# Optimization experiments

Hardware: AMD Instinct MI355X
Metric: run time of the kernel (lower is better)

The kernel has to match this reference:

```python
import jax, jax.numpy as jnp
import numpy as np

N_NODES = 100000
N_GRAPHS = 1000
NPG = 100           # nodes per graph (fixed)
N_EDGES = 3200000   # avg degree 32
F_IN = 128
K = 30              # SortAggregation k
N_CLASSES = 10


def setup_inputs() -> dict:
    key = jax.random.key(0)
    ks = jax.random.split(key, 24)
    x = jax.random.normal(ks[0], (N_NODES, F_IN), jnp.float32)
    # edges constrained within each 100-node graph
    g = jax.random.randint(ks[1], (N_EDGES,), 0, N_GRAPHS)
    src = g * NPG + jax.random.randint(ks[2], (N_EDGES,), 0, NPG)
    dst = g * NPG + jax.random.randint(ks[3], (N_EDGES,), 0, NPG)
    edge_index = jnp.stack([src, dst]).astype(jnp.int32)
    batch = jnp.repeat(jnp.arange(N_GRAPHS, dtype=jnp.int32), NPG)

    def lin(k, fi, fo):
        return jax.random.normal(k, (fi, fo), jnp.float32) / np.sqrt(fi)

    return {
        "x": x, "edge_index": edge_index, "batch": batch,
        "W1": lin(ks[4], F_IN, 32), "b1": jnp.zeros((32,), jnp.float32),
        "W2": lin(ks[5], 32, 32),   "b2": jnp.zeros((32,), jnp.float32),
        "W3": lin(ks[6], 32, 32),   "b3": jnp.zeros((32,), jnp.float32),
        "W4": lin(ks[7], 32, 1),    "b4": jnp.zeros((1,), jnp.float32),
        "conv5_w": jax.random.normal(ks[8], (16, 1, 97), jnp.float32) / np.sqrt(97.0),
        "conv5_b": jnp.zeros((16,), jnp.float32),
        "conv6_w": jax.random.normal(ks[9], (32, 16, 5), jnp.float32) / np.sqrt(16 * 5.0),
        "conv6_b": jnp.zeros((32,), jnp.float32),
        "fc1_w": lin(ks[10], 352, 128), "fc1_b": jnp.zeros((128,), jnp.float32),
        "fc2_w": lin(ks[11], 128, N_CLASSES), "fc2_b": jnp.zeros((N_CLASSES,), jnp.float32),
    }


def reference(x, edge_index, batch,
              W1, b1, W2, b2, W3, b3, W4, b4,
              conv5_w, conv5_b, conv6_w, conv6_b,
              fc1_w, fc1_b, fc2_w, fc2_b):
    N = x.shape[0]
    src, dst = edge_index[0], edge_index[1]
    # remove_self_loops -> zero edge weight; GCNConv then re-adds self loops (weight 1)
    w = jnp.where(src == dst, 0.0, 1.0).astype(x.dtype)
    deg = jax.ops.segment_sum(w, dst, num_segments=N) + 1.0  # includes self loop
    dis = jax.lax.rsqrt(deg)
    norm = w * dis[src] * dis[dst]        # per-edge D^-1/2 A D^-1/2
    self_norm = dis * dis                 # self-loop coefficient 1/deg

    def gcn(h, W, b):
        h = h @ W                                   # [N, out]
        agg = jax.ops.segment_sum(norm[:, None] * h[src], dst, num_segments=N)
        return agg + self_norm[:, None] * h + b

    x1 = jnp.tanh(gcn(x, W1, b1))
    x2 = jnp.tanh(gcn(x1, W2, b2))
    x3 = jnp.tanh(gcn(x2, W3, b3))
    x4 = jnp.tanh(gcn(x3, W4, b4))
    h = jnp.concatenate([x1, x2, x3, x4], axis=-1)  # [N, 97]
    C = h.shape[-1]

    # SortAggregation(k=30): per graph, sort nodes by last channel descending, keep top k
    xs = h.reshape(N_GRAPHS, NPG, C)
    order = jnp.argsort(-xs[..., -1], axis=1)[:, :K]            # [B, K]
    pooled = jnp.take_along_axis(xs, order[:, :, None], axis=1)  # [B, K, C]
    y = pooled.reshape(N_GRAPHS, 1, K * C)                       # [B, 1, 2910]

    dn = ('NCH', 'OIH', 'NCH')
    y = jax.lax.conv_general_dilated(y, conv5_w, (97,), 'VALID', dimension_numbers=dn)
    y = jax.nn.relu(y + conv5_b[None, :, None])                  # [B, 16, 30]
    B, Co, L = y.shape
    y = y.reshape(B, Co, L // 2, 2).max(axis=-1)                 # maxpool(2,2) -> [B,16,15]
    y = jax.lax.conv_general_dilated(y, conv6_w, (1,), 'VALID', dimension_numbers=dn)
    y = jax.nn.relu(y + conv6_b[None, :, None])                  # [B, 32, 11]
    y = y.reshape(B, -1)                                         # [B, 352]
    out = jax.nn.relu(y @ fc1_w + fc1_b)                         # dropout = identity (eval)
    return jax.nn.log_softmax(out @ fc2_w + fc2_b, axis=-1)
```

## Files before the change

kernel.cpp:

```cpp
#include <hip/hip_runtime.h>

#define N_GRAPHS_C 1000
#define NPG_C      100
#define N_EDGES_C  3200000
#define KTOP_C     30
#define CAP        4096
#define NB_BUCKET  391

typedef _Float16 f16x8 __attribute__((ext_vector_type(8)));
typedef float    f32x4 __attribute__((ext_vector_type(4)));

__device__ __forceinline__ unsigned packh2(float x, float y) {
    _Float16 hx = (_Float16)x, hy = (_Float16)y;
    return (unsigned)__builtin_bit_cast(unsigned short, hx) |
           ((unsigned)__builtin_bit_cast(unsigned short, hy) << 16);
}

__device__ __forceinline__ float f16b(unsigned v) {
    return (float)__builtin_bit_cast(_Float16, (unsigned short)v);
}

__device__ __forceinline__ float ftanh(float x) {
    float e = __expf(2.0f * x);
    return 1.0f - 2.0f * __builtin_amdgcn_rcpf(e + 1.0f);
}

__device__ __forceinline__ void split8(const float* v, f16x8& h, f16x8& l) {
    #pragma unroll
    for (int j = 0; j < 8; ++j) {
        _Float16 hh = (_Float16)v[j];
        h[j] = hh;
        l[j] = (_Float16)(v[j] - (float)hh);
    }
}


__global__ __launch_bounds__(1024)
void bucket_kernel(const int* __restrict__ src, const int* __restrict__ dst,
                   int* __restrict__ gcur, unsigned short* __restrict__ slots,
                   const float* __restrict__ W1, const float* __restrict__ W2,
                   const float* __restrict__ W3, unsigned* __restrict__ wp) {
    const int tid = threadIdx.x;
    if (blockIdx.x == NB_BUCKET) {
        for (int w = tid; w < 2048; w += 1024) {
            int n = w >> 6, kp = w & 63, k = kp * 2;
            float a = W1[k*32 + n], b = W1[(k+1)*32 + n];
            _Float16 ah = (_Float16)a, bh = (_Float16)b;
            wp[w]        = (unsigned)__builtin_bit_cast(unsigned short, ah) |
                           ((unsigned)__builtin_bit_cast(unsigned short, bh) << 16);
            wp[2048 + w] = packh2(a - (float)ah, b - (float)bh);
        }
        for (int w = tid; w < 512; w += 1024) {
            int n = w >> 4, kp = w & 15, k = kp * 2;
            float a = W2[k*32 + n], b = W2[(k+1)*32 + n];
            _Float16 ah = (_Float16)a, bh = (_Float16)b;
            wp[4096 + w] = (unsigned)__builtin_bit_cast(unsigned short, ah) |
                           ((unsigned)__builtin_bit_cast(unsigned short, bh) << 16);
            wp[4608 + w] = packh2(a - (float)ah, b - (float)bh);
            float a3 = W3[k*32 + n], b3v = W3[(k+1)*32 + n];
            _Float16 a3h = (_Float16)a3, b3h = (_Float16)b3v;
            wp[5120 + w] = (unsigned)__builtin_bit_cast(unsigned short, a3h) |
                           ((unsigned)__builtin_bit_cast(unsigned short, b3h) << 16);
            wp[5632 + w] = packh2(a3 - (float)a3h, b3v - (float)b3h);
        }
        return;
    }

    __shared__ int hist[N_GRAPHS_C];
    const int base = blockIdx.x * 8192;
    for (int i = tid; i < N_GRAPHS_C; i += 1024) hist[i] = 0;
    __syncthreads();

    int g[8]; unsigned short pk[8]; bool v[8];
    #pragma unroll
    for (int k = 0; k < 8; ++k) {
        int e = base + tid + k * 1024;
        v[k] = false;
        if (e < N_EDGES_C) {
            int s = src[e], d = dst[e];
            if (s != d) {
                int gg = s / NPG_C;
                g[k] = gg;
                pk[k] = (unsigned short)(((d - gg * NPG_C) << 7) | (s - gg * NPG_C));
                v[k] = true;
                atomicAdd(&hist[gg], 1);
            }
        }
    }
    __syncthreads();
    for (int i = tid; i < N_GRAPHS_C; i += 1024) {
        int c = hist[i];
        hist[i] = atomicAdd(&gcur[i], c);
    }
    __syncthreads();
    #pragma unroll
    for (int k = 0; k < 8; ++k) {
        if (v[k]) {
            int pos = atomicAdd(&hist[g[k]], 1);
            if (pos < CAP) slots[g[k] * CAP + pos] = pk[k];
        }
    }
}

#define SMEM_WORDS 8496

extern "C" __global__ __launch_bounds__(512, 8)
void dgcnn_kernel(const float* __restrict__ x,
                  const int* __restrict__ gcur, const unsigned short* __restrict__ slots,
                  const unsigned* __restrict__ wp,
                  const float* __restrict__ b1, const float* __restrict__ b2,
                  const float* __restrict__ b3,
                  const float* __restrict__ W4, const float* __restrict__ b4,
                  const float* __restrict__ w5, const float* __restrict__ b5,
                  const float* __restrict__ w6, const float* __restrict__ b6,
                  const float* __restrict__ fw1, const float* __restrict__ fb1,
                  const float* __restrict__ fw2, const float* __restrict__ fb2,
                  float* __restrict__ out)
{
    extern __shared__ unsigned smu[];
    unsigned* planes = smu;
    unsigned* cnt    = smu + 4352;
    float* xrows  = (float*)(smu + 4352);
    float* pooled = (float*)(smu + 4352);
    float* dis = (float*)(smu + 7952);
    float* t4  = (float*)(smu + 8064);
    unsigned* t4h = smu + 8168;
    unsigned* t4l = smu + 8232;
    float* sX4 = (float*)(smu + 8296);
    int*   srank = (int*)(smu + 8396);
    float* sPb = (float*)smu;
    float* s6  = (float*)smu + 240;
    float* sO1 = (float*)smu + 592;
    float* sFc = (float*)smu + 720;
    float* sZ  = (float*)smu + 1232;

    const int tid = threadIdx.x;
    const int g   = blockIdx.x;
    const int l64 = tid & 63;
    const int wv  = tid >> 6;

    const float* xg = x + (size_t)g * NPG_C * 128;
    const unsigned* w1h = wp;
    const unsigned* w1l = wp + 2048;

    for (int idx = tid; idx < 2600; idx += 512) cnt[idx] = 0u;
    if (tid < 12) dis[100 + tid] = 0.f;
    if (tid < 100) srank[tid] = 0;
    __syncthreads();

    {
        int ec = gcur[g]; if (ec > CAP) ec = CAP;
        for (int k = tid; k < ec; k += 512) {
            unsigned e = slots[g * CAP + k];
            unsigned idx = (e >> 7) * 104 + (e & 127);
            atomicAdd(&cnt[idx >> 2], 1u << ((idx & 3) * 8));
        }
    }
    __syncthreads();

    if (tid < 400) {
        int row = tid >> 2, part = tid & 3;
        int wb = part * 7, we = (part == 3) ? 26 : wb + 7;
        const unsigned* rw = cnt + row * 26;
        unsigned s = 0;
        for (int k = wb; k < we; ++k) {
            unsigned v = rw[k];
            s += (v & 0xffu) + ((v >> 8) & 0xffu) + ((v >> 16) & 0xffu) + (v >> 24);
        }
        atomicAdd(&srank[row], (int)s);
    }
    __syncthreads();

    if (tid < 100) dis[tid] = rsqrtf((float)srank[tid] + 1.0f);
    for (int idx = tid; idx < 768; idx += 512) {
        int rw = idx / 12, wd = idx - rw * 12;
        planes[rw * 68 + 56 + wd] = 0u;
    }
    __syncthreads();

    auto packStore = [&](f32x4 c, int n, int r0, float4 dv) {
        float v0 = c[0]*dv.x, v1 = c[1]*dv.y, v2 = c[2]*dv.z, v3 = c[3]*dv.w;
        _Float16 h0=(_Float16)v0, h1=(_Float16)v1, h2=(_Float16)v2, h3=(_Float16)v3;
        uint2 wh, wl;
        wh.x = (unsigned)__builtin_bit_cast(unsigned short,h0) |
               ((unsigned)__builtin_bit_cast(unsigned short,h1) << 16);
        wh.y = (unsigned)__builtin_bit_cast(unsigned short,h2) |
               ((unsigned)__builtin_bit_cast(unsigned short,h3) << 16);
        wl.x = packh2(v0-(float)h0, v1-(float)h1);
        wl.y = packh2(v2-(float)h2, v3-(float)h3);
        *(uint2*)&planes[n*68 + (r0>>1)] = wh;
        *(uint2*)&planes[2176 + n*68 + (r0>>1)] = wl;
    };

    if (wv < 7) {
        const int arow = (wv << 4) + (l64 & 15);
        const int kq   = (l64 >> 4) << 3;
        const int bn   = l64 & 15;
        const bool aok = arow < 100;
        const int r0 = (wv << 4) + ((l64 >> 4) << 2);
        float4 dv = *(const float4*)&dis[r0];
        #pragma unroll
        for (int t = 0; t < 2; ++t) {
            f32x4 c = {0.f,0.f,0.f,0.f};
            const unsigned* wph = w1h + (bn + 16*t) * 64;
            const unsigned* wpl = w1l + (bn + 16*t) * 64;
            #pragma unroll
            for (int kc = 0; kc < 4; ++kc) {
                const int kb = (kc << 5) + kq;
                f16x8 ah, al;
                if (aok) {
                    float av[8];
                    float4 xa = *(const float4*)&xg[arow*128 + kb];
                    float4 xb = *(const float4*)&xg[arow*128 + kb + 4];
                    av[0]=xa.x; av[1]=xa.y; av[2]=xa.z; av[3]=xa.w;
                    av[4]=xb.x; av[5]=xb.y; av[6]=xb.z; av[7]=xb.w;
                    split8(av, ah, al);
                } else {
                    #pragma unroll
                    for (int j = 0; j < 8; ++j) { ah[j] = (_Float16)0.f; al[j] = (_Float16)0.f; }
                }
                f16x8 bh = __builtin_bit_cast(f16x8, *(const uint4*)(wph + (kb>>1)));
                f16x8 bl = __builtin_bit_cast(f16x8, *(const uint4*)(wpl + (kb>>1)));
                c = __builtin_amdgcn_mfma_f32_16x16x32_f16(ah, bh, c, 0, 0, 0);
                c = __builtin_amdgcn_mfma_f32_16x16x32_f16(al, bh, c, 0, 0, 0);
                c = __builtin_amdgcn_mfma_f32_16x16x32_f16(ah, bl, c, 0, 0, 0);
            }
            packStore(c, bn + 16*t, r0, dv);
        }
    }
    f16x8 afr[4];
    {
        const int arow = (wv << 4) + (l64 & 15);
        if (wv < 7 && arow < 100) {
            const unsigned* cb = cnt + arow * 26 + ((l64 >> 4) << 1);
            #pragma unroll
            for (int ks = 0; ks < 4; ++ks) {
                uint2 cw = *(const uint2*)(cb + ks * 8);
                #pragma unroll
                for (int j = 0; j < 4; ++j) {
                    afr[ks][j]     = (_Float16)(float)((cw.x >> (8*j)) & 255u);
                    afr[ks][4 + j] = (_Float16)(float)((cw.y >> (8*j)) & 255u);
                }
            }
        } else {
            #pragma unroll
            for (int ks = 0; ks < 4; ++ks)
                #pragma unroll
                for (int j = 0; j < 8; ++j) afr[ks][j] = (_Float16)0.f;
        }
    }
    __syncthreads();

    auto AGG = [&](f32x4& fa, f32x4& fb, const float* Bp, bool wx) {
        if (wv < 7) {
            const int n0 = l64 & 15, r0 = (wv << 4) + ((l64 >> 4) << 2);
            const int kw = (l64 >> 4) << 2;
            float4 dv = *(const float4*)&dis[r0];
            #pragma unroll
            for (int t = 0; t < 2; ++t) {
                f32x4 a = {0.f,0.f,0.f,0.f};
                const unsigned* bb = planes + (16*t + n0) * 0 + (n0)*0;
                (void)bb;
                #pragma unroll
                for (int p = 0; p < 2; ++p) {
                    const unsigned* bp = planes + p * 2176 + (16*t + (n0 & 15)) * 0;
                    (void)bp;
                    const unsigned* bq = planes + p * 2176 + ( (t == 0) ? n0 : (16 + n0) ) * 0;
                    (void)bq;
                    const unsigned* br = planes + p * 2176;
                    #pragma unroll
                    for (int ks = 0; ks < 4; ++ks) {
                        f16x8 bfrag = __builtin_bit_cast(f16x8,
                            *(const uint4*)(br + ( (l64 & 15) + 16*t ) * 0 + (l64 & 15) * 68 + 16*t*68 + kw + ks*16));
                        a = __builtin_amdgcn_mfma_f32_16x16x32_f16(afr[ks], bfrag, a, 0, 0, 0);
                    }
                }
                uint2 sh = *(const uint2*)(planes + (16*t + n0) * 68 + (r0 >> 1));
                uint2 sl = *(const uint2*)(planes + 2176 + (16*t + n0) * 68 + (r0 >> 1));
                float bi = Bp[16*t + n0];
                f32x4& fo = t ? fb : fa;
                #pragma unroll
                for (int j = 0; j < 4; ++j) {
                    unsigned sft = (unsigned)((j & 1) * 16);
                    float sc = f16b(((j < 2) ? sh.x : sh.y) >> sft) +
                               f16b(((j < 2) ? sl.x : sl.y) >> sft);
                    float d_ = (j == 0) ? dv.x : (j == 1) ? dv.y : (j == 2) ? dv.z : dv.w;
                    float v = ftanh(d_ * (a[j] + sc) + bi);
                    fo[j] = v;
                    if (wx) {
                        int row = r0 + j;
                        if (row < 100) xrows[row*36 + 16*t + n0] = v;
                    }
                }
            }
        }
    };

    auto XWm = [&](const unsigned* wh, const unsigned* wl) {
        if (wv < 7) {
            const int arow = (wv << 4) + (l64 & 15);
            const int kq   = (l64 >> 4) << 3;
            const int bn   = l64 & 15;
            const int r0 = (wv << 4) + ((l64 >> 4) << 2);
            float4 dv = *(const float4*)&dis[r0];
            f16x8 ah, al;
            if (arow < 100) {
                float av[8];
                float4 xa = *(const float4*)&xrows[arow*36 + kq];
                float4 xb = *(const float4*)&xrows[arow*36 + kq + 4];
                av[0]=xa.x; av[1]=xa.y; av[2]=xa.z; av[3]=xa.w;
                av[4]=xb.x; av[5]=xb.y; av[6]=xb.z; av[7]=xb.w;
                split8(av, ah, al);
            } else {
                #pragma unroll
                for (int j = 0; j < 8; ++j) { ah[j] = (_Float16)0.f; al[j] = (_Float16)0.f; }
            }
            __syncthreads();
            #pragma unroll
            for (int t = 0; t < 2; ++t) {
                f32x4 c = {0.f,0.f,0.f,0.f};
                f16x8 bh = __builtin_bit_cast(f16x8, *(const uint4*)(wh + (bn+16*t)*16 + (kq>>1)));
                f16x8 bl = __builtin_bit_cast(f16x8, *(const uint4*)(wl + (bn+16*t)*16 + (kq>>1)));
                c = __builtin_amdgcn_mfma_f32_16x16x32_f16(ah, bh, c, 0, 0, 0);
                c = __builtin_amdgcn_mfma_f32_16x16x32_f16(al, bh, c, 0, 0, 0);
                c = __builtin_amdgcn_mfma_f32_16x16x32_f16(ah, bl, c, 0, 0, 0);
                packStore(c, bn + 16*t, r0, dv);
            }
        } else {
            __syncthreads();
        }
    };

    f32x4 f1a, f1b, f2a, f2b, f3a, f3b;

    AGG(f1a, f1b, b1, true);
    XWm(wp + 4096, wp + 4608);
    __syncthreads();
    AGG(f2a, f2b, b2, true);
    XWm(wp + 5120, wp + 5632);
    __syncthreads();
    AGG(f3a, f3b, b3, false);

    if (wv < 7) {
        float w4a = W4[l64 & 15], w4b = W4[16 + (l64 & 15)];
        int r0 = (wv << 4) + ((l64 >> 4) << 2);
        #pragma unroll
        for (int j = 0; j < 4; ++j) {
            float v = f3a[j] * w4a + f3b[j] * w4b;
            v += __shfl_xor(v, 1, 16); v += __shfl_xor(v, 2, 16);
            v += __shfl_xor(v, 4, 16); v += __shfl_xor(v, 8, 16);
            int row = r0 + j;
            if ((l64 & 15) == 0 && row < 100) t4[row] = v * dis[row];
        }
    }
    __syncthreads();

    if (tid < 64) {
        float a = (2*tid < 100) ? t4[2*tid] : 0.f;
        float b = (2*tid+1 < 100) ? t4[2*tid+1] : 0.f;
        _Float16 ah = (_Float16)a, bh = (_Float16)b;
        t4h[tid] = (unsigned)__builtin_bit_cast(unsigned short, ah) |
                   ((unsigned)__builtin_bit_cast(unsigned short, bh) << 16);
        t4l[tid] = packh2(a - (float)ah, b - (float)bh);
    }
    if (tid < 100) srank[tid] = 0;
    __syncthreads();

    if (wv < 7) {
        f32x4 c = {0.f,0.f,0.f,0.f};
        const int kq2 = (l64 >> 4) << 2;
        const bool bz = (l64 & 15) == 0;
        #pragma unroll
        for (int ks = 0; ks < 4; ++ks) {
            f16x8 bh, bl;
            if (bz) {
                bh = __builtin_bit_cast(f16x8, *(const uint4*)(t4h + ks*16 + kq2));
                bl = __builtin_bit_cast(f16x8, *(const uint4*)(t4l + ks*16 + kq2));
            } else {
                #pragma unroll
                for (int j = 0; j < 8; ++j) { bh[j] = (_Float16)0.f; bl[j] = (_Float16)0.f; }
            }
            c = __builtin_amdgcn_mfma_f32_16x16x32_f16(afr[ks], bh, c, 0, 0, 0);
            c = __builtin_amdgcn_mfma_f32_16x16x32_f16(afr[ks], bl, c, 0, 0, 0);
        }
        if (bz) {
            int r0 = (wv << 4) + ((l64 >> 4) << 2);
            #pragma unroll
            for (int j = 0; j < 4; ++j) {
                int row = r0 + j;
                if (row < 100) sX4[row] = tanhf(dis[row] * (c[j] + t4[row]) + b4[0]);
            }
        }
    }
    __syncthreads();

    if (tid < 500) {
        int i = tid / 5, seg = tid - i * 5;
        float vi = sX4[i];
        int c = 0, jb = seg * 20;
        #pragma unroll
        for (int jo = 0; jo < 20; ++jo) {
            int j = jb + jo;
            float vj = sX4[j];
            c += (vj > vi) || (vj == vi && j < i);
        }
        atomicAdd(&srank[i], c);
    }
    __syncthreads();

    if (wv < 7) {
        int n0 = l64 & 15, r0 = (wv << 4) + ((l64 >> 4) << 2);
        #pragma unroll
        for (int j = 0; j < 4; ++j) {
            int row = r0 + j;
            if (row < 100) {
                int rk = srank[row];
                if (rk < KTOP_C) {
                    float* pr = pooled + rk * 100;
                    pr[n0]      = f1a[j]; pr[16 + n0] = f1b[j];
                    pr[32 + n0] = f2a[j]; pr[48 + n0] = f2b[j];
                    pr[64 + n0] = f3a[j]; pr[80 + n0] = f3b[j];
                    if (n0 == 0) pr[96] = sX4[row];
                }
            }
        }
    }
    __syncthreads();

    if (tid < 240) {
        int l2 = tid >> 4, co = tid & 15;
        const float* wr = w5 + co * 97;
        float accs[2];
        #pragma unroll
        for (int t = 0; t < 2; ++t) {
            const float* pr = pooled + (2*l2 + t) * 100;
            float acc = b5[co];
            for (int c4 = 0; c4 < 96; c4 += 4) {
                const float4 pv = *(const float4*)&pr[c4];
                acc = fmaf(pv.x, wr[c4+0], fmaf(pv.y, wr[c4+1], fmaf(pv.z, wr[c4+2], fmaf(pv.w, wr[c4+3], acc))));
            }
            accs[t] = fmaf(pr[96], wr[96], acc);
        }
        sPb[co * 15 + l2] = fmaxf(fmaxf(accs[0], accs[1]), 0.f);
    }
    __syncthreads();

    if (tid < 352) {
        int co = tid / 11, l = tid - co * 11;
        float acc = b6[co];
        for (int ci = 0; ci < 16; ++ci) {
            const float* wr = w6 + (co * 16 + ci) * 5;
            const float* pr = sPb + ci * 15 + l;
            acc = fmaf(wr[0], pr[0], fmaf(wr[1], pr[1], fmaf(wr[2], pr[2],
                  fmaf(wr[3], pr[3], fmaf(wr[4], pr[4], acc)))));
        }
        s6[co * 11 + l] = fmaxf(acc, 0.f);
    }
    __syncthreads();

    {
        int j = tid & 127, part = tid >> 7;
        int ibeg = part * 88, iend = ibeg + 88;
        float acc = (part == 0) ? fb1[j] : 0.f;
        for (int i = ibeg; i < iend; ++i)
            acc = fmaf(s6[i], fw1[i * 128 + j], acc);
        sFc[part * 128 + j] = acc;
    }
    __syncthreads();
    if (tid < 128) {
        float v = sFc[tid] + sFc[128 + tid] + sFc[256 + tid] + sFc[384 + tid];
        sO1[tid] = fmaxf(v, 0.f);
    }
    __syncthreads();

    if (tid < 10) {
        float acc = fb2[tid];
        for (int k = 0; k < 128; ++k)
            acc = fmaf(sO1[k], fw2[k * 10 + tid], acc);
        sZ[tid] = acc;
    }
    __syncthreads();
    if (tid < 10) {
        float m = sZ[0];
        for (int c = 1; c < 10; ++c) m = fmaxf(m, sZ[c]);
        float se = 0.f;
        for (int c = 0; c < 10; ++c) se += expf(sZ[c] - m);
        out[g * 10 + tid] = sZ[tid] - m - logf(se);
    }
}

extern "C" void kernel_launch(void* const* d_in, const int* in_sizes, int n_in,
                              void* d_out, int out_size, void* d_ws, size_t ws_size,
                              hipStream_t stream) {
    const float* x   = (const float*)d_in[0];
    const int*   ei  = (const int*)d_in[1];
    const int*   src = ei;
    const int*   dst = ei + N_EDGES_C;
    const float* W1 = (const float*)d_in[3];  const float* b1 = (const float*)d_in[4];
    const float* W2 = (const float*)d_in[5];  const float* b2 = (const float*)d_in[6];
    const float* W3 = (const float*)d_in[7];  const float* b3 = (const float*)d_in[8];
    const float* W4 = (const float*)d_in[9];  const float* b4 = (const float*)d_in[10];
    const float* w5 = (const float*)d_in[11]; const float* b5 = (const float*)d_in[12];
    const float* w6 = (const float*)d_in[13]; const float* b6 = (const float*)d_in[14];
    const float* fw1 = (const float*)d_in[15]; const float* fb1 = (const float*)d_in[16];
    const float* fw2 = (const float*)d_in[17]; const float* fb2 = (const float*)d_in[18];
    float* out = (float*)d_out;

    int* gcur = (int*)d_ws;
    unsigned short* slots = (unsigned short*)((char*)d_ws + 4096);
    unsigned* wpp = (unsigned*)((char*)d_ws + 4096 + (size_t)N_GRAPHS_C * CAP * 2);

    hipMemsetAsync(gcur, 0, 4096, stream);

    bucket_kernel<<<NB_BUCKET + 1, 1024, 0, stream>>>(src, dst, gcur, slots,
                                                      W1, W2, W3, wpp);

    size_t smem = (size_t)SMEM_WORDS * sizeof(unsigned);
    hipFuncSetAttribute((const void*)dgcnn_kernel,
                        hipFuncAttributeMaxDynamicSharedMemorySize, (int)smem);
    dgcnn_kernel<<<N_GRAPHS_C, 512, smem, stream>>>(
        x, gcur, slots, wpp, b1, b2, b3, W4, b4,
        w5, b5, w6, b6, fw1, fb1, fw2, fb2, out);
}
```

Measured before the change: 106.1 us.

## Spill layer-1/2 activations to global scratch and merge W1 MFMA loops

```diff
diff --git a/kernel.cpp b/kernel.cpp
--- a/kernel.cpp
+++ b/kernel.cpp
@@ -108,6 +108,7 @@
 void dgcnn_kernel(const float* __restrict__ x,
                   const int* __restrict__ gcur, const unsigned short* __restrict__ slots,
                   const unsigned* __restrict__ wp,
+                  float* __restrict__ gx1, float* __restrict__ gx2,
                   const float* __restrict__ b1, const float* __restrict__ b2,
                   const float* __restrict__ b3,
                   const float* __restrict__ W4, const float* __restrict__ b4,
@@ -140,8 +141,8 @@
     const int wv  = tid >> 6;
 
     const float* xg = x + (size_t)g * NPG_C * 128;
-    const unsigned* w1h = wp;
-    const unsigned* w1l = wp + 2048;
+    float* gx1b = gx1 + (size_t)g * 3600;
+    float* gx2b = gx2 + (size_t)g * 3600;
 
     for (int idx = tid; idx < 2600; idx += 512) cnt[idx] = 0u;
     if (tid < 12) dis[100 + tid] = 0.f;
@@ -197,36 +198,41 @@
         const int kq   = (l64 >> 4) << 3;
         const int bn   = l64 & 15;
         const bool aok = arow < 100;
+        f32x4 c0 = {0.f,0.f,0.f,0.f}, c1 = {0.f,0.f,0.f,0.f};
+        #pragma unroll
+        for (int kc = 0; kc < 4; ++kc) {
+            const int kb = (kc << 5) + kq;
+            f16x8 ah, al;
+            if (aok) {
+                float av[8];
+                float4 xa = *(const float4*)&xg[arow*128 + kb];
+                float4 xb = *(const float4*)&xg[arow*128 + kb + 4];
+                av[0]=xa.x; av[1]=xa.y; av[2]=xa.z; av[3]=xa.w;
+                av[4]=xb.x; av[5]=xb.y; av[6]=xb.z; av[7]=xb.w;
+                split8(av, ah, al);
+            } else {
+                #pragma unroll
+                for (int j = 0; j < 8; ++j) { ah[j] = (_Float16)0.f; al[j] = (_Float16)0.f; }
+            }
+            {
+                f16x8 bh = __builtin_bit_cast(f16x8, *(const uint4*)(wp + bn*64 + (kb>>1)));
+                f16x8 bl = __builtin_bit_cast(f16x8, *(const uint4*)(wp + 2048 + bn*64 + (kb>>1)));
+                c0 = __builtin_amdgcn_mfma_f32_16x16x32_f16(ah, bh, c0, 0, 0, 0);
+                c0 = __builtin_amdgcn_mfma_f32_16x16x32_f16(al, bh, c0, 0, 0, 0);
+                c0 = __builtin_amdgcn_mfma_f32_16x16x32_f16(ah, bl, c0, 0, 0, 0);
+            }
+            {
+                f16x8 bh = __builtin_bit_cast(f16x8, *(const uint4*)(wp + (bn+16)*64 + (kb>>1)));
+                f16x8 bl = __builtin_bit_cast(f16x8, *(const uint4*)(wp + 2048 + (bn+16)*64 + (kb>>1)));
+                c1 = __builtin_amdgcn_mfma_f32_16x16x32_f16(ah, bh, c1, 0, 0, 0);
+                c1 = __builtin_amdgcn_mfma_f32_16x16x32_f16(al, bh, c1, 0, 0, 0);
+                c1 = __builtin_amdgcn_mfma_f32_16x16x32_f16(ah, bl, c1, 0, 0, 0);
+            }
+        }
         const int r0 = (wv << 4) + ((l64 >> 4) << 2);
         float4 dv = *(const float4*)&dis[r0];
-        #pragma unroll
-        for (int t = 0; t < 2; ++t) {
-            f32x4 c = {0.f,0.f,0.f,0.f};
-            const unsigned* wph = w1h + (bn + 16*t) * 64;
-            const unsigned* wpl = w1l + (bn + 16*t) * 64;
-            #pragma unroll
-            for (int kc = 0; kc < 4; ++kc) {
-                const int kb = (kc << 5) + kq;
-                f16x8 ah, al;
-                if (aok) {
-                    float av[8];
-                    float4 xa = *(const float4*)&xg[arow*128 + kb];
-                    float4 xb = *(const float4*)&xg[arow*128 + kb + 4];
-                    av[0]=xa.x; av[1]=xa.y; av[2]=xa.z; av[3]=xa.w;
-                    av[4]=xb.x; av[5]=xb.y; av[6]=xb.z; av[7]=xb.w;
-                    split8(av, ah, al);
-                } else {
-                    #pragma unroll
-                    for (int j = 0; j < 8; ++j) { ah[j] = (_Float16)0.f; al[j] = (_Float16)0.f; }
-                }
-                f16x8 bh = __builtin_bit_cast(f16x8, *(const uint4*)(wph + (kb>>1)));
-                f16x8 bl = __builtin_bit_cast(f16x8, *(const uint4*)(wpl + (kb>>1)));
-                c = __builtin_amdgcn_mfma_f32_16x16x32_f16(ah, bh, c, 0, 0, 0);
-                c = __builtin_amdgcn_mfma_f32_16x16x32_f16(al, bh, c, 0, 0, 0);
-                c = __builtin_amdgcn_mfma_f32_16x16x32_f16(ah, bl, c, 0, 0, 0);
-            }
-            packStore(c, bn + 16*t, r0, dv);
-        }
+        packStore(c0, bn,      r0, dv);
+        packStore(c1, bn + 16, r0, dv);
     }
     f16x8 afr[4];
     {
@@ -251,7 +257,7 @@
     }
     __syncthreads();
 
-    auto AGG = [&](f32x4& fa, f32x4& fb, const float* Bp, bool wx) {
+    auto AGG = [&](f32x4* fa, f32x4* fb, const float* Bp, bool KEEP) {
         if (wv < 7) {
             const int n0 = l64 & 15, r0 = (wv << 4) + ((l64 >> 4) << 2);
             const int kw = (l64 >> 4) << 2;
@@ -259,26 +265,18 @@
             #pragma unroll
             for (int t = 0; t < 2; ++t) {
                 f32x4 a = {0.f,0.f,0.f,0.f};
-                const unsigned* bb = planes + (16*t + n0) * 0 + (n0)*0;
-                (void)bb;
                 #pragma unroll
                 for (int p = 0; p < 2; ++p) {
-                    const unsigned* bp = planes + p * 2176 + (16*t + (n0 & 15)) * 0;
-                    (void)bp;
-                    const unsigned* bq = planes + p * 2176 + ( (t == 0) ? n0 : (16 + n0) ) * 0;
-                    (void)bq;
-                    const unsigned* br = planes + p * 2176;
+                    const unsigned* bp = planes + p * 2176 + (16*t + n0) * 68 + kw;
                     #pragma unroll
                     for (int ks = 0; ks < 4; ++ks) {
-                        f16x8 bfrag = __builtin_bit_cast(f16x8,
-                            *(const uint4*)(br + ( (l64 & 15) + 16*t ) * 0 + (l64 & 15) * 68 + 16*t*68 + kw + ks*16));
+                        f16x8 bfrag = __builtin_bit_cast(f16x8, *(const uint4*)(bp + ks*16));
                         a = __builtin_amdgcn_mfma_f32_16x16x32_f16(afr[ks], bfrag, a, 0, 0, 0);
                     }
                 }
                 uint2 sh = *(const uint2*)(planes + (16*t + n0) * 68 + (r0 >> 1));
                 uint2 sl = *(const uint2*)(planes + 2176 + (16*t + n0) * 68 + (r0 >> 1));
                 float bi = Bp[16*t + n0];
-                f32x4& fo = t ? fb : fa;
                 #pragma unroll
                 for (int j = 0; j < 4; ++j) {
                     unsigned sft = (unsigned)((j & 1) * 16);
@@ -286,8 +284,8 @@
                                f16b(((j < 2) ? sl.x : sl.y) >> sft);
                     float d_ = (j == 0) ? dv.x : (j == 1) ? dv.y : (j == 2) ? dv.z : dv.w;
                     float v = ftanh(d_ * (a[j] + sc) + bi);
-                    fo[j] = v;
-                    if (wx) {
+                    if (KEEP) { (t ? *fb : *fa)[j] = v; }
+                    else {
                         int row = r0 + j;
                         if (row < 100) xrows[row*36 + 16*t + n0] = v;
                     }
@@ -296,7 +294,7 @@
         }
     };
 
-    auto XWm = [&](const unsigned* wh, const unsigned* wl) {
+    auto XWm = [&](const unsigned* wh, const unsigned* wl, float* gxb) {
         if (wv < 7) {
             const int arow = (wv << 4) + (l64 & 15);
             const int kq   = (l64 >> 4) << 3;
@@ -315,7 +313,6 @@
                 #pragma unroll
                 for (int j = 0; j < 8; ++j) { ah[j] = (_Float16)0.f; al[j] = (_Float16)0.f; }
             }
-            __syncthreads();
             #pragma unroll
             for (int t = 0; t < 2; ++t) {
                 f32x4 c = {0.f,0.f,0.f,0.f};
@@ -326,20 +323,21 @@
                 c = __builtin_amdgcn_mfma_f32_16x16x32_f16(ah, bl, c, 0, 0, 0);
                 packStore(c, bn + 16*t, r0, dv);
             }
-        } else {
-            __syncthreads();
-        }
+        }
+        for (int idx = tid; idx < 3600; idx += 512) gxb[idx] = xrows[idx];
     };
 
-    f32x4 f1a, f1b, f2a, f2b, f3a, f3b;
-
-    AGG(f1a, f1b, b1, true);
-    XWm(wp + 4096, wp + 4608);
-    __syncthreads();
-    AGG(f2a, f2b, b2, true);
-    XWm(wp + 5120, wp + 5632);
-    __syncthreads();
-    AGG(f3a, f3b, b3, false);
+    f32x4 f3a, f3b;
+
+    AGG(nullptr, nullptr, b1, false);
+    __syncthreads();
+    XWm(wp + 4096, wp + 4608, gx1b);
+    __syncthreads();
+    AGG(nullptr, nullptr, b2, false);
+    __syncthreads();
+    XWm(wp + 5120, wp + 5632, gx2b);
+    __syncthreads();
+    AGG(&f3a, &f3b, b3, true);
 
     if (wv < 7) {
         float w4a = W4[l64 & 15], w4b = W4[16 + (l64 & 15)];
@@ -417,9 +415,12 @@
                 int rk = srank[row];
                 if (rk < KTOP_C) {
                     float* pr = pooled + rk * 100;
-                    pr[n0]      = f1a[j]; pr[16 + n0] = f1b[j];
-                    pr[32 + n0] = f2a[j]; pr[48 + n0] = f2b[j];
-                    pr[64 + n0] = f3a[j]; pr[80 + n0] = f3b[j];
+                    pr[n0]      = gx1b[row*36 + n0];
+                    pr[16 + n0] = gx1b[row*36 + 16 + n0];
+                    pr[32 + n0] = gx2b[row*36 + n0];
+                    pr[48 + n0] = gx2b[row*36 + 16 + n0];
+                    pr[64 + n0] = f3a[j];
+                    pr[80 + n0] = f3b[j];
                     if (n0 == 0) pr[96] = sX4[row];
                 }
             }
@@ -509,6 +510,8 @@
     int* gcur = (int*)d_ws;
     unsigned short* slots = (unsigned short*)((char*)d_ws + 4096);
     unsigned* wpp = (unsigned*)((char*)d_ws + 4096 + (size_t)N_GRAPHS_C * CAP * 2);
+    float* gx1 = (float*)((char*)d_ws + 4096 + (size_t)N_GRAPHS_C * CAP * 2 + 24576);
+    float* gx2 = gx1 + (size_t)N_GRAPHS_C * 3600;
 
     hipMemsetAsync(gcur, 0, 4096, stream);
 
@@ -519,6 +522,6 @@
     hipFuncSetAttribute((const void*)dgcnn_kernel,
                         hipFuncAttributeMaxDynamicSharedMemorySize, (int)smem);
     dgcnn_kernel<<<N_GRAPHS_C, 512, smem, stream>>>(
-        x, gcur, slots, wpp, b1, b2, b3, W4, b4,
+        x, gcur, slots, wpp, gx1, gx2, b1, b2, b3, W4, b4,
         w5, b5, w6, b6, fw1, fb1, fw2, fb2, out);
 }
```

Result: faster. 103.7 us (-2.2%).
